# Kernel tuning notes

Measured on AMD Instinct MI355X. Metric: run time of the kernel, lower is better.

## Reference

```python
import jax, jax.numpy as jnp
import numpy as np

NUM_NODES = 50000

def _gat_conv(x, edge_index, W, a_src, a_dst, b):
    # PyG GATConv, heads=1: h = x W ; e_ij = LeakyReLU(a_src.h_j + a_dst.h_i)
    # softmax over incoming edges of i ; out_i = sum_j alpha_ij h_j + b
    h = x @ W                                  # [N, F]
    src, dst = edge_index[0], edge_index[1]    # edge j->i : src=j, dst=i
    alpha_s = h @ a_src                        # [N]
    alpha_d = h @ a_dst                        # [N]
    e = jax.nn.leaky_relu(alpha_s[src] + alpha_d[dst], negative_slope=0.2)  # [E]
    # segment softmax over destination nodes
    e_max = jax.ops.segment_max(e, dst, num_segments=NUM_NODES)
    e_exp = jnp.exp(e - e_max[dst])
    denom = jax.ops.segment_sum(e_exp, dst, num_segments=NUM_NODES)
    coef = e_exp / denom[dst]                  # [E]
    out = jax.ops.segment_sum(h[src] * coef[:, None], dst, num_segments=NUM_NODES)
    return out + b

def setup_inputs() -> dict:
    key = jax.random.key(0)
    ks = jax.random.split(key, 10)
    N, E, IN, HID, OUT = NUM_NODES, 800000, 256, 256, 128
    x = jax.random.normal(ks[0], (N, IN), dtype=jnp.float32)
    edge_index = jax.random.randint(ks[1], (2, E), 0, N, dtype=jnp.int32)
    def glorot(k, shape):
        lim = float(np.sqrt(6.0 / (shape[0] + shape[-1])))
        return jax.random.uniform(k, shape, jnp.float32, -lim, lim)
    return {
        'x': x,
        'edge_index': edge_index,
        'W1': glorot(ks[2], (IN, HID)),
        'a_src1': glorot(ks[3], (HID,)),
        'a_dst1': glorot(ks[4], (HID,)),
        'b1': jnp.zeros((HID,), jnp.float32),
        'W2': glorot(ks[5], (HID, OUT)),
        'a_src2': glorot(ks[6], (OUT,)),
        'a_dst2': glorot(ks[7], (OUT,)),
        'b2': jnp.zeros((OUT,), jnp.float32),
    }

def reference(x, edge_index, W1, a_src1, a_dst1, b1, W2, a_src2, a_dst2, b2):
    # add self loops once (same edge_index used by both convs)
    ar = jnp.arange(NUM_NODES, dtype=edge_index.dtype)
    ei = jnp.concatenate([edge_index, jnp.stack([ar, ar])], axis=1)
    x1 = _gat_conv(x, ei, W1, a_src1, a_dst1, b1)
    h = jax.nn.relu(x1)          # dropout p=0.3 is identity in eval mode
    x2 = _gat_conv(h, ei, W2, a_src2, a_dst2, b2)
    return (x2, h)
```

## Files before the change

### kernel.cpp

```cpp
#include <hip/hip_runtime.h>
#include <hip/hip_bf16.h>

#define N_NODES 50000
#define E0      800000
#define ETOT    850000

typedef __bf16 bf16x8 __attribute__((ext_vector_type(8)));
typedef float  f32x4  __attribute__((ext_vector_type(4)));
typedef ushort u16x8  __attribute__((ext_vector_type(8)));
union B8 { u16x8 u; bf16x8 b; };

static __device__ __forceinline__ float b2f(ushort u) {
    union { uint u; float f; } x; x.u = ((uint)u) << 16; return x.f;
}
static __device__ __forceinline__ ushort f2bf(float f) {
    uint u = __builtin_bit_cast(uint, f);
    uint r = (u + 0x7FFFu + ((u >> 16) & 1u)) >> 16;
    return (ushort)r;
}


__global__ __launch_bounds__(256) void k_deg(const int* __restrict__ ei, int* __restrict__ deg) {
    int e = blockIdx.x * 256 + threadIdx.x;
    if (e >= ETOT) return;
    int dst = (e < E0) ? ei[E0 + e] : (e - E0);
    atomicAdd(&deg[dst], 1);
}

__global__ __launch_bounds__(256) void k_scan1(const int* __restrict__ deg, int* __restrict__ offs,
                                               int* __restrict__ bsum) {
    __shared__ int buf[256];
    int tid = threadIdx.x;
    int i = blockIdx.x * 256 + tid;
    int v = (i < N_NODES) ? deg[i] : 0;
    buf[tid] = v;
    __syncthreads();
    for (int off = 1; off < 256; off <<= 1) {
        int t = (tid >= off) ? buf[tid - off] : 0;
        __syncthreads();
        buf[tid] += t;
        __syncthreads();
    }
    if (i < N_NODES) offs[i + 1] = buf[tid];
    if (tid == 255) bsum[blockIdx.x] = buf[255];
}

__global__ __launch_bounds__(256) void k_scan2(int* __restrict__ bsum, int nb) {
    __shared__ int buf[256];
    int tid = threadIdx.x;
    int v = (tid < nb) ? bsum[tid] : 0;
    buf[tid] = v;
    __syncthreads();
    for (int off = 1; off < 256; off <<= 1) {
        int t = (tid >= off) ? buf[tid - off] : 0;
        __syncthreads();
        buf[tid] += t;
        __syncthreads();
    }
    if (tid < nb) bsum[tid] = buf[tid] - v;
}

__global__ __launch_bounds__(256) void k_scan3(int* __restrict__ offs, const int* __restrict__ bsum,
                                               int* __restrict__ cursor) {
    int tid = threadIdx.x;
    int i = blockIdx.x * 256 + tid;
    if (i < N_NODES) {
        int v = offs[i + 1] + bsum[blockIdx.x];
        offs[i + 1] = v;
        cursor[i + 1] = v;
    }
    if (i == 0) { offs[0] = 0; cursor[0] = 0; }
}

__global__ __launch_bounds__(256) void k_scatter(const int* __restrict__ ei, int* __restrict__ cursor,
                                                 int* __restrict__ esrc) {
    int e = blockIdx.x * 256 + threadIdx.x;
    if (e >= ETOT) return;
    int src, dst;
    if (e < E0) { src = ei[e]; dst = ei[E0 + e]; }
    else        { src = e - E0; dst = src; }
    int pos = atomicAdd(&cursor[dst], 1);
    esrc[pos] = src;
}

__global__ __launch_bounds__(256) void k_splitT(const float* __restrict__ W, ushort* __restrict__ th,
                                                ushort* __restrict__ tl, int K, int N) {
    int i = blockIdx.x * 256 + threadIdx.x;
    if (i >= K * N) return;
    int n = i / K, k = i - n * K;
    float v = W[(size_t)k * N + n];
    ushort h = f2bf(v);
    th[(size_t)n * K + k] = h;
    tl[(size_t)n * K + k] = f2bf(v - b2f(h));
}

__global__ __launch_bounds__(256) void k_wvec(const float* __restrict__ W1, const float* __restrict__ s1v,
                                              const float* __restrict__ d1v, const float* __restrict__ W2,
                                              const float* __restrict__ s2v, const float* __restrict__ d2v,
                                              float* __restrict__ w1s, float* __restrict__ w1d,
                                              float* __restrict__ w2s, float* __restrict__ w2d) {
    int gw = (blockIdx.x * 256 + threadIdx.x) >> 6;
    int lane = threadIdx.x & 63;
    int vec = gw >> 8, kk = gw & 255;
    float a = 0.f;
    if (vec == 0)      { for (int n = lane; n < 256; n += 64) a += W1[(size_t)kk * 256 + n] * s1v[n]; }
    else if (vec == 1) { for (int n = lane; n < 256; n += 64) a += W1[(size_t)kk * 256 + n] * d1v[n]; }
    else if (vec == 2) { for (int n = lane; n < 128; n += 64) a += W2[(size_t)kk * 128 + n] * s2v[n]; }
    else               { for (int n = lane; n < 128; n += 64) a += W2[(size_t)kk * 128 + n] * d2v[n]; }
    for (int o = 32; o; o >>= 1) a += __shfl_down(a, o);
    if (lane == 0) {
        if (vec == 0) w1s[kk] = a;
        else if (vec == 1) w1d[kk] = a;
        else if (vec == 2) w2s[kk] = a;
        else w2d[kk] = a;
    }
}

__global__ __launch_bounds__(256) void k_prep1(const float* __restrict__ x, const float* __restrict__ w1s,
                                               const float* __restrict__ w1d, ushort* __restrict__ xb,
                                               float* __restrict__ as1, float* __restrict__ ad1) {
    int gw = (blockIdx.x * 256 + threadIdx.x) >> 6;
    int lane = threadIdx.x & 63;
    if (gw >= N_NODES) return;
    float4 v = *(const float4*)(x + (size_t)gw * 256 + lane * 4);
    ushort4 h;
    h.x = f2bf(v.x); h.y = f2bf(v.y); h.z = f2bf(v.z); h.w = f2bf(v.w);
    *(ushort4*)(xb + (size_t)gw * 256 + lane * 4) = h;
    float4 cs = *(const float4*)(w1s + lane * 4);
    float4 cd = *(const float4*)(w1d + lane * 4);
    float s = v.x * cs.x + v.y * cs.y + v.z * cs.z + v.w * cs.w;
    float d = v.x * cd.x + v.y * cd.y + v.z * cd.z + v.w * cd.w;
    for (int o = 32; o; o >>= 1) { s += __shfl_down(s, o); d += __shfl_down(d, o); }
    if (lane == 0) { as1[gw] = s; ad1[gw] = d; }
}


__global__ __launch_bounds__(256, 2) void k_gemm_mfma(const ushort* __restrict__ Ab,
                                                      const ushort* __restrict__ Bth,
                                                      const ushort* __restrict__ Btl,
                                                      ushort* __restrict__ Cb, int M, int Nn) {
    constexpr int K = 256;
    __shared__ ushort lds[2][2][8][128][8];
    int tid = threadIdx.x;
    int wid = tid >> 6, lane = tid & 63;
    int wr = wid >> 1, wc = wid & 1;
    int bm = blockIdx.x * 128, bn = blockIdx.y * 128;
    int lr = lane & 15, lg = lane >> 4;

    int sa = tid >> 7, scol = tid & 127;
    const ushort* sb = (sa ? Btl : Bth) + (size_t)(bn + scol) * K;

    const ushort* Ap[4];
#pragma unroll
    for (int m = 0; m < 4; ++m) {
        int row = bm + wr * 64 + m * 16 + lr;
        if (row >= M) row = M - 1;
        Ap[m] = Ab + (size_t)row * K + lg * 8;
    }

    f32x4 acc[4][4] = {};
    u16x8 sv[8];
    bf16x8 aH[2][4];

#pragma unroll
    for (int c = 0; c < 8; ++c) sv[c] = *(const u16x8*)(sb + c * 8);
#pragma unroll
    for (int m = 0; m < 4; ++m) {
        aH[0][m] = *(const bf16x8*)(Ap[m]);
        aH[1][m] = *(const bf16x8*)(Ap[m] + 32);
    }
#pragma unroll
    for (int c = 0; c < 8; ++c) *(u16x8*)&lds[0][sa][c][scol][0] = sv[c];
    __syncthreads();

#pragma unroll
    for (int s = 0; s < 8; ++s) {
        const int w = s >> 1, buf = w & 1, kk = s & 1;
        if (kk == 0 && w < 3) {
#pragma unroll
            for (int c = 0; c < 8; ++c) sv[c] = *(const u16x8*)(sb + (w + 1) * 64 + c * 8);
        }
        bf16x8 bh[4], bl[4];
#pragma unroll
        for (int n = 0; n < 4; ++n) {
            int col = wc * 64 + n * 16 + lr;
            B8 th, tl2;
            th.u = *(const u16x8*)&lds[buf][0][kk * 4 + lg][col][0];
            tl2.u = *(const u16x8*)&lds[buf][1][kk * 4 + lg][col][0];
            bh[n] = th.b; bl[n] = tl2.b;
        }
        bf16x8 ah[4];
#pragma unroll
        for (int m = 0; m < 4; ++m) ah[m] = aH[s & 1][m];
        if (s < 6) {
#pragma unroll
            for (int m = 0; m < 4; ++m) aH[s & 1][m] = *(const bf16x8*)(Ap[m] + (s + 2) * 32);
        }
#pragma unroll
        for (int m = 0; m < 4; ++m)
#pragma unroll
            for (int n = 0; n < 4; ++n) {
                acc[m][n] = __builtin_amdgcn_mfma_f32_16x16x32_bf16(ah[m], bh[n], acc[m][n], 0, 0, 0);
                acc[m][n] = __builtin_amdgcn_mfma_f32_16x16x32_bf16(ah[m], bl[n], acc[m][n], 0, 0, 0);
            }
        if (kk == 1 && w < 3) {
#pragma unroll
            for (int c = 0; c < 8; ++c) *(u16x8*)&lds[buf ^ 1][sa][c][scol][0] = sv[c];
            __syncthreads();
        }
    }
#pragma unroll
    for (int m = 0; m < 4; ++m)
#pragma unroll
        for (int r = 0; r < 4; ++r) {
            int row = bm + wr * 64 + m * 16 + lg * 4 + r;
            if (row < M) {
#pragma unroll
                for (int n = 0; n < 4; ++n) {
                    int col = bn + wc * 64 + n * 16 + lr;
                    Cb[(size_t)row * Nn + col] = f2bf(acc[m][n][r]);
                }
            }
        }
}

template <int F, bool RELU, bool WB, bool A2>
__global__ __launch_bounds__(256) void k_aggf(const int* __restrict__ offs, const int* __restrict__ esrc,
                                              const float* __restrict__ as, const float* __restrict__ ad,
                                              const ushort* __restrict__ H, const float* __restrict__ bias,
                                              float* __restrict__ out, ushort* __restrict__ hb,
                                              const float* __restrict__ w2s, const float* __restrict__ w2d,
                                              float* __restrict__ as2, float* __restrict__ ad2) {
    constexpr int V = F / 64;
    constexpr float THR = 8.f;
    int gw = (blockIdx.x * 256 + threadIdx.x) >> 6;
    int lane = threadIdx.x & 63;
    if (gw >= N_NODES) return;
    int s0 = offs[gw], s1 = offs[gw + 1];
    float adi = ad[gw];
    float m = -1e30f, ssum = 0.f;
    float acc[V] = {};
    int k = s0;
    for (; k + 7 < s1; k += 8) {
        int rr[8];
#pragma unroll
        for (int q = 0; q < 8; ++q) rr[q] = esrc[k + q];
        float ev[8];
#pragma unroll
        for (int q = 0; q < 8; ++q) ev[q] = as[rr[q]];
        float rows[8][V];
#pragma unroll
        for (int q = 0; q < 8; ++q) {
            if constexpr (V == 4) {
                ushort4 v = *(const ushort4*)(H + (size_t)rr[q] * F + lane * 4);
                rows[q][0] = b2f(v.x); rows[q][1] = b2f(v.y); rows[q][2] = b2f(v.z); rows[q][3] = b2f(v.w);
            } else {
                ushort2 v = *(const ushort2*)(H + (size_t)rr[q] * F + lane * 2);
                rows[q][0] = b2f(v.x); rows[q][1] = b2f(v.y);
            }
        }
        float em = -1e30f;
#pragma unroll
        for (int q = 0; q < 8; ++q) {
            float e = ev[q] + adi;
            e = e > 0.f ? e : 0.2f * e;
            ev[q] = e;
            em = fmaxf(em, e);
        }
        if (em > m + THR) {
            float sc = __expf(m - em);
            ssum *= sc;
#pragma unroll
            for (int j = 0; j < V; ++j) acc[j] *= sc;
            m = em;
        }
        float w[8];
#pragma unroll
        for (int q = 0; q < 8; ++q) w[q] = __expf(ev[q] - m);
#pragma unroll
        for (int q = 0; q < 8; ++q) ssum += w[q];
#pragma unroll
        for (int j = 0; j < V; ++j) {
            float a = acc[j];
#pragma unroll
            for (int q = 0; q < 8; ++q) a += w[q] * rows[q][j];
            acc[j] = a;
        }
    }
    for (; k + 3 < s1; k += 4) {
        int rr[4];
#pragma unroll
        for (int q = 0; q < 4; ++q) rr[q] = esrc[k + q];
        float ev[4];
#pragma unroll
        for (int q = 0; q < 4; ++q) ev[q] = as[rr[q]];
        float rows[4][V];
#pragma unroll
        for (int q = 0; q < 4; ++q) {
            if constexpr (V == 4) {
                ushort4 v = *(const ushort4*)(H + (size_t)rr[q] * F + lane * 4);
                rows[q][0] = b2f(v.x); rows[q][1] = b2f(v.y); rows[q][2] = b2f(v.z); rows[q][3] = b2f(v.w);
            } else {
                ushort2 v = *(const ushort2*)(H + (size_t)rr[q] * F + lane * 2);
                rows[q][0] = b2f(v.x); rows[q][1] = b2f(v.y);
            }
        }
        float em = -1e30f;
#pragma unroll
        for (int q = 0; q < 4; ++q) {
            float e = ev[q] + adi;
            e = e > 0.f ? e : 0.2f * e;
            ev[q] = e;
            em = fmaxf(em, e);
        }
        if (em > m + THR) {
            float sc = __expf(m - em);
            ssum *= sc;
#pragma unroll
            for (int j = 0; j < V; ++j) acc[j] *= sc;
            m = em;
        }
        float w[4];
#pragma unroll
        for (int q = 0; q < 4; ++q) w[q] = __expf(ev[q] - m);
#pragma unroll
        for (int q = 0; q < 4; ++q) ssum += w[q];
#pragma unroll
        for (int j = 0; j < V; ++j) {
            float a = acc[j];
#pragma unroll
            for (int q = 0; q < 4; ++q) a += w[q] * rows[q][j];
            acc[j] = a;
        }
    }
    for (; k < s1; ++k) {
        int r0 = esrc[k];
        float row0[V];
        if constexpr (V == 4) {
            ushort4 v0 = *(const ushort4*)(H + (size_t)r0 * F + lane * 4);
            row0[0] = b2f(v0.x); row0[1] = b2f(v0.y); row0[2] = b2f(v0.z); row0[3] = b2f(v0.w);
        } else {
            ushort2 v0 = *(const ushort2*)(H + (size_t)r0 * F + lane * 2);
            row0[0] = b2f(v0.x); row0[1] = b2f(v0.y);
        }
        float e0 = as[r0] + adi; e0 = e0 > 0.f ? e0 : 0.2f * e0;
        if (e0 > m + THR) {
            float sc = __expf(m - e0);
            ssum *= sc;
#pragma unroll
            for (int j = 0; j < V; ++j) acc[j] *= sc;
            m = e0;
        }
        float w0 = __expf(e0 - m);
        ssum += w0;
#pragma unroll
        for (int j = 0; j < V; ++j) acc[j] += w0 * row0[j];
    }
    float inv = 1.f / ssum;
    float r[V];
#pragma unroll
    for (int j = 0; j < V; ++j) {
        r[j] = acc[j] * inv + bias[lane * V + j];
        if (RELU) r[j] = fmaxf(r[j], 0.f);
    }
    if (V == 4) *(float4*)(out + (size_t)gw * F + lane * 4) = make_float4(r[0], r[1], r[2], r[3]);
    else        *(float2*)(out + (size_t)gw * F + lane * 2) = make_float2(r[0], r[1]);
    if constexpr (WB && V == 4) {
        ushort4 h4;
        h4.x = f2bf(r[0]); h4.y = f2bf(r[1]); h4.z = f2bf(r[2]); h4.w = f2bf(r[3]);
        *(ushort4*)(hb + (size_t)gw * F + lane * 4) = h4;
    }
    if constexpr (A2 && V == 4) {
        float4 cs = *(const float4*)(w2s + lane * 4);
        float4 cd = *(const float4*)(w2d + lane * 4);
        float s2 = r[0] * cs.x + r[1] * cs.y + r[2] * cs.z + r[3] * cs.w;
        float d2 = r[0] * cd.x + r[1] * cd.y + r[2] * cd.z + r[3] * cd.w;
        for (int o = 32; o; o >>= 1) { s2 += __shfl_down(s2, o); d2 += __shfl_down(d2, o); }
        if (lane == 0) { as2[gw] = s2; ad2[gw] = d2; }
    }
}


static inline size_t al256(size_t x) { return (x + 255) & ~(size_t)255; }

extern "C" void kernel_launch(void* const* d_in, const int* in_sizes, int n_in,
                              void* d_out, int out_size, void* d_ws, size_t ws_size,
                              hipStream_t stream) {
    const float* x   = (const float*)d_in[0];
    const int*   ei  = (const int*)d_in[1];
    const float* W1  = (const float*)d_in[2];
    const float* as1 = (const float*)d_in[3];
    const float* ad1 = (const float*)d_in[4];
    const float* b1  = (const float*)d_in[5];
    const float* W2  = (const float*)d_in[6];
    const float* as2 = (const float*)d_in[7];
    const float* ad2 = (const float*)d_in[8];
    const float* b2  = (const float*)d_in[9];

    float* out_x2 = (float*)d_out;
    float* out_h  = (float*)d_out + (size_t)N_NODES * 128;

    const size_t NM256 = (size_t)N_NODES * 256 * 2;
    char* base = (char*)d_ws;
    size_t off = 0;
    auto take = [&](size_t bytes) { char* p = base + off; off = al256(off + bytes); return p; };

    ushort* h1b  = (ushort*)take(NM256);
    ushort* xb   = (ushort*)take(NM256);
    ushort* hb   = (ushort*)take(NM256);
    ushort* w1th = (ushort*)take(256 * 256 * 2);
    ushort* w1tl = (ushort*)take(256 * 256 * 2);
    ushort* w2th = (ushort*)take(256 * 128 * 2);
    ushort* w2tl = (ushort*)take(256 * 128 * 2);
    float*  w1s  = (float*)take(256 * 4);
    float*  w1d  = (float*)take(256 * 4);
    float*  w2s  = (float*)take(256 * 4);
    float*  w2d  = (float*)take(256 * 4);
    float*  a1s  = (float*)take(N_NODES * 4);
    float*  a1d  = (float*)take(N_NODES * 4);
    float*  a2s  = (float*)take(N_NODES * 4);
    float*  a2d  = (float*)take(N_NODES * 4);
    int*    deg  = (int*)take(N_NODES * 4);
    int*    offs = (int*)take((N_NODES + 4) * 4);
    int*    curs = (int*)take((N_NODES + 4) * 4);
    int*    bsum = (int*)take(1024);
    int*    esrc = (int*)take((size_t)ETOT * 4);
    (void)ws_size;

    hipMemsetAsync(deg, 0, N_NODES * sizeof(int), stream);

    int nbE = (ETOT + 255) / 256;
    int nbN = (N_NODES + 255) / 256;
    int nbW = (N_NODES * 64 + 255) / 256;

    k_deg<<<nbE, 256, 0, stream>>>(ei, deg);
    k_scan1<<<nbN, 256, 0, stream>>>(deg, offs, bsum);
    k_scan2<<<1, 256, 0, stream>>>(bsum, nbN);
    k_scan3<<<nbN, 256, 0, stream>>>(offs, bsum, curs);
    k_scatter<<<nbE, 256, 0, stream>>>(ei, curs, esrc);

    k_splitT<<<(256 * 256 + 255) / 256, 256, 0, stream>>>(W1, w1th, w1tl, 256, 256);
    k_splitT<<<(256 * 128 + 255) / 256, 256, 0, stream>>>(W2, w2th, w2tl, 256, 128);
    k_wvec<<<256, 256, 0, stream>>>(W1, as1, ad1, W2, as2, ad2, w1s, w1d, w2s, w2d);
    k_prep1<<<nbW, 256, 0, stream>>>(x, w1s, w1d, xb, a1s, a1d);

    dim3 g1((N_NODES + 127) / 128, 2), g2((N_NODES + 127) / 128, 1);

    k_gemm_mfma<<<g1, 256, 0, stream>>>(xb, w1th, w1tl, h1b, N_NODES, 256);
    k_aggf<256, true, true, true><<<nbW, 256, 0, stream>>>(offs, esrc, a1s, a1d, h1b, b1,
                                                           out_h, hb, w2s, w2d, a2s, a2d);

    ushort* gb = h1b;
    k_gemm_mfma<<<g2, 256, 0, stream>>>(hb, w2th, w2tl, gb, N_NODES, 128);
    k_aggf<128, false, false, false><<<nbW, 256, 0, stream>>>(offs, esrc, a2s, a2d, gb, b2,
                                                              out_x2, nullptr, nullptr, nullptr,
                                                              nullptr, nullptr);
}
```

Measured before the change: 289.5 us.

## Stage GEMM A and B tiles via direct global-to-LDS loads with double buffering

Rewrites the bf16 MFMA GEMM so both the A and B (hi/lo split) tiles are copied straight from global memory into double-buffered LDS using global_load_lds. This replaces register-staged B copies and per-lane direct A loads. A single barrier per k-step replaces the earlier staging scheme, and occupancy is raised to 3 blocks per SM. The A input buffers are padded by one tile so out-of-range rows read valid memory instead of being clamped. Risks include LDS bank conflicts from the unpadded [128][32] layout, and whether the barrier properly waits on async LDS loads (vmcnt).

```diff
diff --git a/kernel.cpp b/kernel.cpp
--- a/kernel.cpp
+++ b/kernel.cpp
@@ -17,6 +17,11 @@
     uint u = __builtin_bit_cast(uint, f);
     uint r = (u + 0x7FFFu + ((u >> 16) & 1u)) >> 16;
     return (ushort)r;
+}
+
+static __device__ __forceinline__ void gload16(const ushort* g, ushort* l) {
+    __builtin_amdgcn_global_load_lds((const __attribute__((address_space(1))) unsigned int*)g,
+                                     (__attribute__((address_space(3))) unsigned int*)l, 16, 0, 0);
 }
 
 
@@ -135,66 +140,53 @@
 }
 
 
-__global__ __launch_bounds__(256, 2) void k_gemm_mfma(const ushort* __restrict__ Ab,
+__global__ __launch_bounds__(256, 3) void k_gemm_mfma(const ushort* __restrict__ Ab,
                                                       const ushort* __restrict__ Bth,
                                                       const ushort* __restrict__ Btl,
                                                       ushort* __restrict__ Cb, int M, int Nn) {
     constexpr int K = 256;
-    __shared__ ushort lds[2][2][8][128][8];
+    __shared__ ushort ldsA[2][128][32];
+    __shared__ ushort ldsB[2][2][128][32];
     int tid = threadIdx.x;
     int wid = tid >> 6, lane = tid & 63;
     int wr = wid >> 1, wc = wid & 1;
     int bm = blockIdx.x * 128, bn = blockIdx.y * 128;
     int lr = lane & 15, lg = lane >> 4;
 
-    int sa = tid >> 7, scol = tid & 127;
-    const ushort* sb = (sa ? Btl : Bth) + (size_t)(bn + scol) * K;
-
-    const ushort* Ap[4];
-#pragma unroll
-    for (int m = 0; m < 4; ++m) {
-        int row = bm + wr * 64 + m * 16 + lr;
-        if (row >= M) row = M - 1;
-        Ap[m] = Ab + (size_t)row * K + lg * 8;
-    }
+    int srow = tid >> 2, sk = (tid & 3) << 3;
+    const ushort* ga0  = Ab  + (size_t)(bm + srow) * K + sk;
+    const ushort* ga1  = Ab  + (size_t)(bm + srow + 64) * K + sk;
+    const ushort* gbh0 = Bth + (size_t)(bn + srow) * K + sk;
+    const ushort* gbh1 = Bth + (size_t)(bn + srow + 64) * K + sk;
+    const ushort* gbl0 = Btl + (size_t)(bn + srow) * K + sk;
+    const ushort* gbl1 = Btl + (size_t)(bn + srow + 64) * K + sk;
+
+#define STAGE(B, KT) do {                                   \
+    gload16(ga0  + (KT), &ldsA[B][srow][sk]);               \
+    gload16(ga1  + (KT), &ldsA[B][srow + 64][sk]);          \
+    gload16(gbh0 + (KT), &ldsB[B][0][srow][sk]);            \
+    gload16(gbh1 + (KT), &ldsB[B][0][srow + 64][sk]);       \
+    gload16(gbl0 + (KT), &ldsB[B][1][srow][sk]);            \
+    gload16(gbl1 + (KT), &ldsB[B][1][srow + 64][sk]);       \
+} while (0)
 
     f32x4 acc[4][4] = {};
-    u16x8 sv[8];
-    bf16x8 aH[2][4];
-
-#pragma unroll
-    for (int c = 0; c < 8; ++c) sv[c] = *(const u16x8*)(sb + c * 8);
-#pragma unroll
-    for (int m = 0; m < 4; ++m) {
-        aH[0][m] = *(const bf16x8*)(Ap[m]);
-        aH[1][m] = *(const bf16x8*)(Ap[m] + 32);
-    }
-#pragma unroll
-    for (int c = 0; c < 8; ++c) *(u16x8*)&lds[0][sa][c][scol][0] = sv[c];
+
+    STAGE(0, 0);
     __syncthreads();
 
 #pragma unroll
     for (int s = 0; s < 8; ++s) {
-        const int w = s >> 1, buf = w & 1, kk = s & 1;
-        if (kk == 0 && w < 3) {
-#pragma unroll
-            for (int c = 0; c < 8; ++c) sv[c] = *(const u16x8*)(sb + (w + 1) * 64 + c * 8);
-        }
-        bf16x8 bh[4], bl[4];
+        const int buf = s & 1;
+        if (s < 7) STAGE(buf ^ 1, (s + 1) * 32);
+        bf16x8 ah[4], bh[4], bl[4];
+#pragma unroll
+        for (int m = 0; m < 4; ++m)
+            ah[m] = *(const bf16x8*)&ldsA[buf][wr * 64 + m * 16 + lr][lg * 8];
 #pragma unroll
         for (int n = 0; n < 4; ++n) {
-            int col = wc * 64 + n * 16 + lr;
-            B8 th, tl2;
-            th.u = *(const u16x8*)&lds[buf][0][kk * 4 + lg][col][0];
-            tl2.u = *(const u16x8*)&lds[buf][1][kk * 4 + lg][col][0];
-            bh[n] = th.b; bl[n] = tl2.b;
-        }
-        bf16x8 ah[4];
-#pragma unroll
-        for (int m = 0; m < 4; ++m) ah[m] = aH[s & 1][m];
-        if (s < 6) {
-#pragma unroll
-            for (int m = 0; m < 4; ++m) aH[s & 1][m] = *(const bf16x8*)(Ap[m] + (s + 2) * 32);
+            bh[n] = *(const bf16x8*)&ldsB[buf][0][wc * 64 + n * 16 + lr][lg * 8];
+            bl[n] = *(const bf16x8*)&ldsB[buf][1][wc * 64 + n * 16 + lr][lg * 8];
         }
 #pragma unroll
         for (int m = 0; m < 4; ++m)
@@ -203,12 +195,9 @@
                 acc[m][n] = __builtin_amdgcn_mfma_f32_16x16x32_bf16(ah[m], bh[n], acc[m][n], 0, 0, 0);
                 acc[m][n] = __builtin_amdgcn_mfma_f32_16x16x32_bf16(ah[m], bl[n], acc[m][n], 0, 0, 0);
             }
-        if (kk == 1 && w < 3) {
-#pragma unroll
-            for (int c = 0; c < 8; ++c) *(u16x8*)&lds[buf ^ 1][sa][c][scol][0] = sv[c];
-            __syncthreads();
-        }
-    }
+        __syncthreads();
+    }
+#undef STAGE
 #pragma unroll
     for (int m = 0; m < 4; ++m)
 #pragma unroll
@@ -401,13 +390,14 @@
     float* out_h  = (float*)d_out + (size_t)N_NODES * 128;
 
     const size_t NM256 = (size_t)N_NODES * 256 * 2;
+    const size_t PAD   = (size_t)128 * 256 * 2;
     char* base = (char*)d_ws;
     size_t off = 0;
     auto take = [&](size_t bytes) { char* p = base + off; off = al256(off + bytes); return p; };
 
     ushort* h1b  = (ushort*)take(NM256);
-    ushort* xb   = (ushort*)take(NM256);
-    ushort* hb   = (ushort*)take(NM256);
+    ushort* xb   = (ushort*)take(NM256 + PAD);
+    ushort* hb   = (ushort*)take(NM256 + PAD);
     ushort* w1th = (ushort*)take(256 * 256 * 2);
     ushort* w1tl = (ushort*)take(256 * 256 * 2);
     ushort* w2th = (ushort*)take(256 * 128 * 2);
```

Measured after the change: 272.7 us. 1.06x faster.
